# Optimization experiments

Measured on AMD Instinct MI355X. Metric: run time of the kernel, lower is better.

The kernel has to match this reference:

```python
import jax, jax.numpy as jnp
import numpy as np


def setup_inputs() -> dict:
    key = jax.random.key(0)
    ks = jax.random.split(key, 5)
    B, T, D, L = 4, 8192, 1024, 128
    X = jax.random.normal(ks[0], (B, T, D), dtype=jnp.float32)
    attention_mask = jnp.ones((B, T), dtype=jnp.float32)
    sd_dl = 1.0 / np.sqrt(D)  # lecun_normal fan_in = D
    Wk = jax.random.normal(ks[1], (D, L), dtype=jnp.float32) * sd_dl
    Wq = jax.random.normal(ks[2], (D, L), dtype=jnp.float32) * sd_dl
    Wv = jax.random.normal(ks[3], (D, D), dtype=jnp.float32) * sd_dl
    o_proj = jax.random.normal(ks[4], (D, D), dtype=jnp.float32) * sd_dl
    return {"X": X, "attention_mask": attention_mask, "Wk": Wk, "Wq": Wq,
            "Wv": Wv, "o_proj": o_proj, "n_heads": 16}


def reference(X, attention_mask, Wk, Wq, Wv, o_proj, n_heads):
    B, T, D = X.shape
    H = n_heads
    # Projections, laid out time-major as in the original: (T, B, H, *)
    V = jnp.einsum('DM,BTD->TBM', Wv, X).reshape(T, B, H, -1)   # (T,B,H,d)
    Q = jnp.einsum('DL,BTD->TBL', Wq, X).reshape(T, B, H, -1)   # (T,B,H,l)
    K = jnp.einsum('DL,BTD->TBL', Wk, X).reshape(T, B, H, -1)   # (T,B,H,l)
    m = attention_mask.T[:, :, None, None]                       # (T,B,1,1)
    V = V * m
    Qs = jax.nn.softmax(Q, axis=-1)
    maxi = jnp.max(K, axis=0, keepdims=True)                     # global max over T
    K = jnp.exp(K - maxi) * m
    Kv = jnp.einsum('tbhl,tbhd->bhld', K, V)                     # global KV state
    Ksum = K.sum(axis=0)                                         # (B,H,l)
    Kv = Kv / Ksum[..., None]
    y = jnp.einsum('tbhl,bhld->bthd', Qs, Kv).reshape(B, T, D)
    return y @ o_proj
```

## Files before the change

kernel.cpp:

```cpp
#include <hip/hip_runtime.h>
#include <hip/hip_bf16.h>

typedef unsigned short u16;
typedef unsigned int   u32;

typedef __attribute__((ext_vector_type(8))) short short8;
typedef __attribute__((ext_vector_type(4))) float f32x4;

typedef const __attribute__((address_space(1))) void g_void;
typedef __attribute__((address_space(3))) void l_void;

__device__ __forceinline__ float bf2f(u16 u) {
    u32 x = ((u32)u) << 16;
    return __builtin_bit_cast(float, x);
}
__device__ __forceinline__ u16 f2bf(float f) {
    u32 u = __builtin_bit_cast(u32, f);
    u32 r = (u + 0x7FFFu + ((u >> 16) & 1u)) >> 16;
    return (u16)r;
}
__device__ __forceinline__ u32 pack2(float a, float b) {
    return (u32)f2bf(a) | ((u32)f2bf(b) << 16);
}

__global__ void detect_kernel(const u16* __restrict__ X, int* __restrict__ flags) {
    __shared__ int cnt[256];
    int c = 0;
    for (int i = threadIdx.x; i < 16384; i += 256) {
        u16 v = X[i];
        int e = (v >> 7) & 0xFF;
        c += (e >= 104 && e <= 140) ? 1 : 0;
    }
    cnt[threadIdx.x] = c;
    __syncthreads();
    for (int s = 128; s > 0; s >>= 1) {
        if (threadIdx.x < s) cnt[threadIdx.x] += cnt[threadIdx.x + s];
        __syncthreads();
    }
    if (threadIdx.x == 0) {
        flags[0] = (cnt[0] < 14746) ? 1 : 0;
        flags[1] = 0;
    }
}

__global__ __launch_bounds__(256) void convert_x(const float* __restrict__ Xf,
                                                 u16* __restrict__ XC,
                                                 const int* __restrict__ flags, int n) {
    if (flags[0] == 0) return;
    int i = (blockIdx.x * 256 + threadIdx.x) * 8;
    if (i >= n) return;
    float4 a = *(const float4*)(Xf + i);
    float4 b = *(const float4*)(Xf + i + 4);
    uint4 o;
    o.x = pack2(a.x, a.y); o.y = pack2(a.z, a.w);
    o.z = pack2(b.x, b.y); o.w = pack2(b.z, b.w);
    *(uint4*)(XC + i) = o;
}

__global__ __launch_bounds__(256) void gemm_bt(
    const u16* __restrict__ A0, const u16* __restrict__ A1, int lda,
    const u16* __restrict__ Bt, int ldb,
    void* __restrict__ C, int ldc,
    int Mtiles, int K,
    const int* __restrict__ aselp, const int* __restrict__ ofp) {
    __shared__ char smem[32768];

    const u16* A = aselp[0] ? A1 : A0;

    const int tid = threadIdx.x;
    const int w = tid >> 6, lane = tid & 63;
    const int Ntiles = gridDim.x / Mtiles;
    const int q8 = gridDim.x >> 3;
    const int t  = (blockIdx.x & 7) * q8 + (blockIdx.x >> 3);
    const int mt = t / Ntiles;
    const int nt = t % Ntiles;
    const int m0 = mt << 7, n0 = nt << 7;
    const int wm = w >> 1, wn = w & 1;

    f32x4 acc[4][4] = {};

    const int rr = w * 16 + (lane >> 2);
    const int cg = (lane & 3) ^ ((lane >> 3) & 3);

    const u16* gA0 = A + (m0 + rr) * lda + cg * 8;
    const u16* gA1 = A + (m0 + rr + 64) * lda + cg * 8;
    const u16* gB0 = Bt + (n0 + rr) * ldb + cg * 8;
    const u16* gB1 = Bt + (n0 + rr + 64) * ldb + cg * 8;

    const int st0 = w * 1024 + lane * 16;

    const int fr_a = (wm << 6) + (lane & 15);
    const int fr_b = (wn << 6) + (lane & 15);
    const int sl = (lane >> 4) ^ ((lane >> 1) & 3);
    const int offA = fr_a * 64 + sl * 16;
    const int offB = 8192 + fr_b * 64 + sl * 16;

#define STAGE(buf, kt) do {                                                        \
        char* sb_ = smem + (buf) * 16384;                                          \
        __builtin_amdgcn_global_load_lds((g_void*)(gA0 + (kt)),                    \
            (l_void*)(sb_ + st0), 16, 0, 0);                                       \
        __builtin_amdgcn_global_load_lds((g_void*)(gA1 + (kt)),                    \
            (l_void*)(sb_ + 4096 + st0), 16, 0, 0);                                \
        __builtin_amdgcn_global_load_lds((g_void*)(gB0 + (kt)),                    \
            (l_void*)(sb_ + 8192 + st0), 16, 0, 0);                                \
        __builtin_amdgcn_global_load_lds((g_void*)(gB1 + (kt)),                    \
            (l_void*)(sb_ + 12288 + st0), 16, 0, 0);                               \
    } while (0)

#define COMPUTE(buf) do {                                                          \
        const char* cb_ = smem + (buf) * 16384;                                    \
        short8 af[4], bfv[4];                                                      \
        _Pragma("unroll")                                                          \
        for (int i = 0; i < 4; ++i) {                                              \
            af[i]  = *(const short8*)(cb_ + offA + i * 1024);                      \
            bfv[i] = *(const short8*)(cb_ + offB + i * 1024);                      \
        }                                                                          \
        _Pragma("unroll")                                                          \
        for (int mi = 0; mi < 4; ++mi)                                             \
            _Pragma("unroll")                                                      \
            for (int ni = 0; ni < 4; ++ni)                                         \
                acc[mi][ni] = __builtin_amdgcn_mfma_f32_16x16x32_bf16(             \
                    af[mi], bfv[ni], acc[mi][ni], 0, 0, 0);                        \
    } while (0)

    STAGE(0, 0);
    int cur = 0;
    for (int kt = 32; kt < K; kt += 32) {
        STAGE(cur ^ 1, kt);
        asm volatile("s_waitcnt vmcnt(4)" ::: "memory");
        __builtin_amdgcn_s_barrier();
        __builtin_amdgcn_sched_barrier(0);
        COMPUTE(cur);
        __builtin_amdgcn_sched_barrier(0);
        __builtin_amdgcn_s_barrier();
        cur ^= 1;
    }
    asm volatile("s_waitcnt vmcnt(0)" ::: "memory");
    __builtin_amdgcn_s_barrier();
    __builtin_amdgcn_sched_barrier(0);
    COMPUTE(cur);
    __syncthreads();

#undef STAGE
#undef COMPUTE

    const int out_fp32 = ofp[0];
    float* fb = (float*)smem;
    const int lrow = tid >> 3, cgp = tid & 7;
#pragma unroll
    for (int mi = 0; mi < 4; ++mi) {
#pragma unroll
        for (int ni = 0; ni < 4; ++ni) {
#pragma unroll
            for (int r = 0; r < 4; ++r) {
                int lr = wm * 16 + ((lane >> 4) << 2) + r;
                int lc = wn * 64 + ni * 16 + (lane & 15);
                fb[lr * 132 + lc] = acc[mi][ni][r];
            }
        }
        __syncthreads();
        int grow = (lrow < 16) ? (mi * 16 + lrow) : (48 + mi * 16 + lrow);
        const float* srcp = fb + lrow * 132 + cgp * 16;
        if (out_fp32) {
            float4* dst = (float4*)((float*)C + (size_t)(m0 + grow) * ldc + n0 + cgp * 16);
            dst[0] = make_float4(srcp[0], srcp[1], srcp[2], srcp[3]);
            dst[1] = make_float4(srcp[4], srcp[5], srcp[6], srcp[7]);
            dst[2] = make_float4(srcp[8], srcp[9], srcp[10], srcp[11]);
            dst[3] = make_float4(srcp[12], srcp[13], srcp[14], srcp[15]);
        } else {
            u32 o0 = pack2(srcp[0], srcp[1]);
            u32 o1 = pack2(srcp[2], srcp[3]);
            u32 o2 = pack2(srcp[4], srcp[5]);
            u32 o3 = pack2(srcp[6], srcp[7]);
            u32 o4 = pack2(srcp[8], srcp[9]);
            u32 o5 = pack2(srcp[10], srcp[11]);
            u32 o6 = pack2(srcp[12], srcp[13]);
            u32 o7 = pack2(srcp[14], srcp[15]);
            uint4* dst = (uint4*)((u16*)C + (size_t)(m0 + grow) * ldc + n0 + cgp * 16);
            dst[0] = make_uint4(o0, o1, o2, o3);
            dst[1] = make_uint4(o4, o5, o6, o7);
        }
        __syncthreads();
    }
}

__device__ __forceinline__ u16 rd_elem(const void* s, int idx, int fp32) {
    return fp32 ? f2bf(((const float*)s)[idx]) : ((const u16*)s)[idx];
}

__global__ void transpose_k(const void* __restrict__ Wq, const void* __restrict__ Wk,
                            const void* __restrict__ Wv, const void* __restrict__ Op,
                            u16* __restrict__ W1T, u16* __restrict__ OpT,
                            const int* __restrict__ flags) {
    int fp32 = flags[0];
    int id = blockIdx.x;
    const void* src; u16* dst; int Nc, mid;
    if (id < 128)       { src = Wq; dst = W1T;               Nc = 128;  mid = id; }
    else if (id < 256)  { src = Wk; dst = W1T + 128 * 1024;  Nc = 128;  mid = id - 128; }
    else if (id < 1280) { src = Wv; dst = W1T + 256 * 1024;  Nc = 1024; mid = id - 256; }
    else                { src = Op; dst = OpT;               Nc = 1024; mid = id - 1280; }
    int kt = mid & 31, nt = mid >> 5;
    __shared__ u16 tile[32][33];
    int x = threadIdx.x & 31, y0 = threadIdx.x >> 5;
#pragma unroll
    for (int yy = 0; yy < 4; ++yy) {
        int y = y0 * 4 + yy;
        tile[y][x] = rd_elem(src, (kt * 32 + y) * Nc + nt * 32 + x, fp32);
    }
    __syncthreads();
#pragma unroll
    for (int yy = 0; yy < 4; ++yy) {
        int y = y0 * 4 + yy;
        dst[(nt * 32 + y) * 1024 + kt * 32 + x] = tile[x][y];
    }
}

__global__ __launch_bounds__(256) void kvpart_kernel(const u16* __restrict__ QKV,
                                                     const void* __restrict__ mask,
                                                     const int* __restrict__ flags,
                                                     float* __restrict__ Kvp,
                                                     float* __restrict__ Ksp) {
    int t_ = (blockIdx.x & 7) * 256 + (blockIdx.x >> 3);
    int h = t_ & 15;
    int bc = t_ >> 4;
    int chunk = bc & 31, b = bc >> 5;
    int w = threadIdx.x >> 6, lane = threadIdx.x & 63;
    int fp32m = flags[0];

    float kv[8] = {0, 0, 0, 0, 0, 0, 0, 0};
    float ks[8] = {0, 0, 0, 0, 0, 0, 0, 0};
    int t0 = chunk * 256;
    for (int i = 0; i < 64; ++i) {
        int t = t0 + w + i * 4;
        int m = b * 8192 + t;
        const u16* row = QKV + (size_t)m * 1280;
        float v = bf2f(row[256 + h * 64 + lane]);
        uint4 kq = *(const uint4*)(row + 128 + h * 8);
        float msk = fp32m ? ((const float*)mask)[m] : bf2f(((const u16*)mask)[m]);
        float vm = v * msk;
        float kf[8];
        kf[0] = __builtin_bit_cast(float, kq.x << 16);
        kf[1] = __builtin_bit_cast(float, kq.x & 0xffff0000u);
        kf[2] = __builtin_bit_cast(float, kq.y << 16);
        kf[3] = __builtin_bit_cast(float, kq.y & 0xffff0000u);
        kf[4] = __builtin_bit_cast(float, kq.z << 16);
        kf[5] = __builtin_bit_cast(float, kq.z & 0xffff0000u);
        kf[6] = __builtin_bit_cast(float, kq.w << 16);
        kf[7] = __builtin_bit_cast(float, kq.w & 0xffff0000u);
#pragma unroll
        for (int l = 0; l < 8; ++l) {
            float e = __expf(kf[l]) * msk;
            kv[l] += e * vm;
            ks[l] += e;
        }
    }
    __shared__ float red[4][8][64];
    __shared__ float redks[4][8];
#pragma unroll
    for (int l = 0; l < 8; ++l) red[w][l][lane] = kv[l];
    if (lane == 0) {
#pragma unroll
        for (int l = 0; l < 8; ++l) redks[w][l] = ks[l];
    }
    __syncthreads();
    int tid = threadIdx.x;
    int obid = (b * 16 + h) * 32 + chunk;
    for (int c = tid; c < 512; c += 256) {
        int l = c >> 6, d = c & 63;
        Kvp[obid * 512 + c] = red[0][l][d] + red[1][l][d] + red[2][l][d] + red[3][l][d];
    }
    if (tid < 8) Ksp[obid * 8 + tid] = redks[0][tid] + redks[1][tid] + redks[2][tid] + redks[3][tid];
}

__global__ void kvreduce_kernel(const float* __restrict__ Kvp, const float* __restrict__ Ksp,
                                float* __restrict__ Kv) {
    int bh = blockIdx.x >> 2;
    int seg = blockIdx.x & 3;
    int c0 = seg * 128 + threadIdx.x;
    int l = c0 >> 6;
    float s = 0.f, ks = 0.f;
    for (int c = 0; c < 32; ++c) {
        s += Kvp[(bh * 32 + c) * 512 + c0];
        ks += Ksp[(bh * 32 + c) * 8 + l];
    }
    Kv[bh * 512 + c0] = s / ks;
}

__global__ __launch_bounds__(256) void y_kernel(u16* __restrict__ QKV,
                                                const float* __restrict__ Kv) {
    int bid = blockIdx.x;
    int b = bid >> 9, chunk = bid & 511;
    int w = threadIdx.x >> 6, lane = threadIdx.x & 63;
    int hh = w & 1;
    int rp = w >> 1;
    int hloc = lane >> 3;
    int h = hh * 8 + hloc;
    int dg = lane & 7;

    float4 kva[8], kvb[8];
    const float* kvp = Kv + (b * 16 + h) * 512 + dg * 8;
#pragma unroll
    for (int l = 0; l < 8; ++l) {
        kva[l] = *(const float4*)(kvp + l * 64);
        kvb[l] = *(const float4*)(kvp + l * 64 + 4);
    }
    int lgrp = lane & 56;
    for (int i = 0; i < 8; ++i) {
        int t = chunk * 16 + i * 2 + rp;
        int m = b * 8192 + t;
        u16* row = QKV + (size_t)m * 1280;
        float qv = bf2f(row[hh * 64 + lane]);
        float qm = qv;
        qm = fmaxf(qm, __shfl_xor(qm, 1));
        qm = fmaxf(qm, __shfl_xor(qm, 2));
        qm = fmaxf(qm, __shfl_xor(qm, 4));
        float e = __expf(qv - qm);
        float s = e;
        s += __shfl_xor(s, 1);
        s += __shfl_xor(s, 2);
        s += __shfl_xor(s, 4);
        float qs = e / s;
        float4 a0 = {0.f, 0.f, 0.f, 0.f}, a1 = {0.f, 0.f, 0.f, 0.f};
#pragma unroll
        for (int l = 0; l < 8; ++l) {
            float ql = __shfl(qs, lgrp + l);
            a0.x += ql * kva[l].x; a0.y += ql * kva[l].y;
            a0.z += ql * kva[l].z; a0.w += ql * kva[l].w;
            a1.x += ql * kvb[l].x; a1.y += ql * kvb[l].y;
            a1.z += ql * kvb[l].z; a1.w += ql * kvb[l].w;
        }
        uint4 o;
        o.x = pack2(a0.x, a0.y);
        o.y = pack2(a0.z, a0.w);
        o.z = pack2(a1.x, a1.y);
        o.w = pack2(a1.z, a1.w);
        *(uint4*)(row + 256 + h * 64 + dg * 8) = o;
    }
}

#define OFF_FLAG ((size_t)0)
#define OFF_W1T  ((size_t)1024)
#define OFF_OPT  ((size_t)2622464)
#define OFF_KVP  ((size_t)4787200)
#define OFF_KSP  ((size_t)8981504)
#define OFF_KV   ((size_t)9047040)
#define OFF_XC   ((size_t)9309184)
#define OFF_QKV  ((size_t)76418048)

extern "C" void kernel_launch(void* const* d_in, const int* in_sizes, int n_in,
                              void* d_out, int out_size, void* d_ws, size_t ws_size,
                              hipStream_t stream) {
    const u16* X   = (const u16*)d_in[0];
    const void* msk = d_in[1];
    const void* Wk  = d_in[2];
    const void* Wq  = d_in[3];
    const void* Wv  = d_in[4];
    const void* Op  = d_in[5];

    char* ws = (char*)d_ws;
    int*   FLAGS = (int*)(ws + OFF_FLAG);
    u16*   W1T  = (u16*)(ws + OFF_W1T);
    u16*   OPT  = (u16*)(ws + OFF_OPT);
    float* KVP  = (float*)(ws + OFF_KVP);
    float* KSP  = (float*)(ws + OFF_KSP);
    float* KV   = (float*)(ws + OFF_KV);
    u16*   XC   = (u16*)(ws + OFF_XC);
    u16*   QKV  = (u16*)(ws + OFF_QKV);

    detect_kernel<<<1, 256, 0, stream>>>(X, FLAGS);
    convert_x<<<16384, 256, 0, stream>>>((const float*)d_in[0], XC, FLAGS, 33554432);
    transpose_k<<<2304, 256, 0, stream>>>(Wq, Wk, Wv, Op, W1T, OPT, FLAGS);
    gemm_bt<<<2560, 256, 0, stream>>>(X, XC, 1024, W1T, 1024, QKV, 1280, 256, 1024,
                                      FLAGS, FLAGS + 1);
    kvpart_kernel<<<2048, 256, 0, stream>>>(QKV, msk, FLAGS, KVP, KSP);
    kvreduce_kernel<<<256, 128, 0, stream>>>(KVP, KSP, KV);
    y_kernel<<<2048, 256, 0, stream>>>(QKV, KV);
    gemm_bt<<<2048, 256, 0, stream>>>(QKV + 256, QKV + 256, 1280, OPT, 1024,
                                      d_out, 1024, 256, 1024, FLAGS + 1, FLAGS);
}
```

Baseline: 533.9 us.

## Triple-buffer GEMM K-loop and merge X conversion with weight transpose kernel

```diff
diff --git a/kernel.cpp b/kernel.cpp
--- a/kernel.cpp
+++ b/kernel.cpp
@@ -43,18 +43,48 @@
     }
 }
 
-__global__ __launch_bounds__(256) void convert_x(const float* __restrict__ Xf,
-                                                 u16* __restrict__ XC,
-                                                 const int* __restrict__ flags, int n) {
-    if (flags[0] == 0) return;
-    int i = (blockIdx.x * 256 + threadIdx.x) * 8;
-    if (i >= n) return;
-    float4 a = *(const float4*)(Xf + i);
-    float4 b = *(const float4*)(Xf + i + 4);
-    uint4 o;
-    o.x = pack2(a.x, a.y); o.y = pack2(a.z, a.w);
-    o.z = pack2(b.x, b.y); o.w = pack2(b.z, b.w);
-    *(uint4*)(XC + i) = o;
+__device__ __forceinline__ u16 rd_elem(const void* s, int idx, int fp32) {
+    return fp32 ? f2bf(((const float*)s)[idx]) : ((const u16*)s)[idx];
+}
+
+__global__ __launch_bounds__(256) void prep_kernel(
+    const float* __restrict__ Xf, u16* __restrict__ XC,
+    const void* __restrict__ Wq, const void* __restrict__ Wk,
+    const void* __restrict__ Wv, const void* __restrict__ Op,
+    u16* __restrict__ W1T, u16* __restrict__ OpT,
+    const int* __restrict__ flags) {
+    int fp32 = flags[0];
+    if (blockIdx.x < 16384) {
+        if (fp32 == 0) return;
+        int i = (blockIdx.x * 256 + threadIdx.x) * 8;
+        float4 a = *(const float4*)(Xf + i);
+        float4 b = *(const float4*)(Xf + i + 4);
+        uint4 o;
+        o.x = pack2(a.x, a.y); o.y = pack2(a.z, a.w);
+        o.z = pack2(b.x, b.y); o.w = pack2(b.z, b.w);
+        *(uint4*)(XC + i) = o;
+        return;
+    }
+    int id = blockIdx.x - 16384;
+    const void* src; u16* dst; int Nc, mid;
+    if (id < 128)       { src = Wq; dst = W1T;               Nc = 128;  mid = id; }
+    else if (id < 256)  { src = Wk; dst = W1T + 128 * 1024;  Nc = 128;  mid = id - 128; }
+    else if (id < 1280) { src = Wv; dst = W1T + 256 * 1024;  Nc = 1024; mid = id - 256; }
+    else                { src = Op; dst = OpT;               Nc = 1024; mid = id - 1280; }
+    int kt = mid & 31, nt = mid >> 5;
+    __shared__ u16 tile[32][33];
+    int x = threadIdx.x & 31, y0 = threadIdx.x >> 5;
+#pragma unroll
+    for (int yy = 0; yy < 4; ++yy) {
+        int y = y0 * 4 + yy;
+        tile[y][x] = rd_elem(src, (kt * 32 + y) * Nc + nt * 32 + x, fp32);
+    }
+    __syncthreads();
+#pragma unroll
+    for (int yy = 0; yy < 4; ++yy) {
+        int y = y0 * 4 + yy;
+        dst[(nt * 32 + y) * 1024 + kt * 32 + x] = tile[x][y];
+    }
 }
 
 __global__ __launch_bounds__(256) void gemm_bt(
@@ -63,7 +93,7 @@
     void* __restrict__ C, int ldc,
     int Mtiles, int K,
     const int* __restrict__ aselp, const int* __restrict__ ofp) {
-    __shared__ char smem[32768];
+    __shared__ char smem[49152];
 
     const u16* A = aselp[0] ? A1 : A0;
 
@@ -123,22 +153,32 @@
                     af[mi], bfv[ni], acc[mi][ni], 0, 0, 0);                        \
     } while (0)
 
+    const int ntiles = K >> 5;
     STAGE(0, 0);
-    int cur = 0;
-    for (int kt = 32; kt < K; kt += 32) {
-        STAGE(cur ^ 1, kt);
-        asm volatile("s_waitcnt vmcnt(4)" ::: "memory");
+    STAGE(1, 32);
+    int cc = 0, sc = 2;
+    for (int i = 0; i < ntiles - 2; ++i) {
+        STAGE(sc, (i + 2) << 5);
+        asm volatile("s_waitcnt vmcnt(8)" ::: "memory");
         __builtin_amdgcn_s_barrier();
         __builtin_amdgcn_sched_barrier(0);
-        COMPUTE(cur);
+        COMPUTE(cc);
         __builtin_amdgcn_sched_barrier(0);
         __builtin_amdgcn_s_barrier();
-        cur ^= 1;
-    }
+        cc = (cc == 2) ? 0 : cc + 1;
+        sc = (sc == 2) ? 0 : sc + 1;
+    }
+    asm volatile("s_waitcnt vmcnt(4)" ::: "memory");
+    __builtin_amdgcn_s_barrier();
+    __builtin_amdgcn_sched_barrier(0);
+    COMPUTE(cc);
+    __builtin_amdgcn_sched_barrier(0);
+    __builtin_amdgcn_s_barrier();
+    cc = (cc == 2) ? 0 : cc + 1;
     asm volatile("s_waitcnt vmcnt(0)" ::: "memory");
     __builtin_amdgcn_s_barrier();
     __builtin_amdgcn_sched_barrier(0);
-    COMPUTE(cur);
+    COMPUTE(cc);
     __syncthreads();
 
 #undef STAGE
@@ -184,37 +224,6 @@
     }
 }
 
-__device__ __forceinline__ u16 rd_elem(const void* s, int idx, int fp32) {
-    return fp32 ? f2bf(((const float*)s)[idx]) : ((const u16*)s)[idx];
-}
-
-__global__ void transpose_k(const void* __restrict__ Wq, const void* __restrict__ Wk,
-                            const void* __restrict__ Wv, const void* __restrict__ Op,
-                            u16* __restrict__ W1T, u16* __restrict__ OpT,
-                            const int* __restrict__ flags) {
-    int fp32 = flags[0];
-    int id = blockIdx.x;
-    const void* src; u16* dst; int Nc, mid;
-    if (id < 128)       { src = Wq; dst = W1T;               Nc = 128;  mid = id; }
-    else if (id < 256)  { src = Wk; dst = W1T + 128 * 1024;  Nc = 128;  mid = id - 128; }
-    else if (id < 1280) { src = Wv; dst = W1T + 256 * 1024;  Nc = 1024; mid = id - 256; }
-    else                { src = Op; dst = OpT;               Nc = 1024; mid = id - 1280; }
-    int kt = mid & 31, nt = mid >> 5;
-    __shared__ u16 tile[32][33];
-    int x = threadIdx.x & 31, y0 = threadIdx.x >> 5;
-#pragma unroll
-    for (int yy = 0; yy < 4; ++yy) {
-        int y = y0 * 4 + yy;
-        tile[y][x] = rd_elem(src, (kt * 32 + y) * Nc + nt * 32 + x, fp32);
-    }
-    __syncthreads();
-#pragma unroll
-    for (int yy = 0; yy < 4; ++yy) {
-        int y = y0 * 4 + yy;
-        dst[(nt * 32 + y) * 1024 + kt * 32 + x] = tile[x][y];
-    }
-}
-
 __global__ __launch_bounds__(256) void kvpart_kernel(const u16* __restrict__ QKV,
                                                      const void* __restrict__ mask,
                                                      const int* __restrict__ flags,
@@ -368,8 +377,8 @@
     u16*   QKV  = (u16*)(ws + OFF_QKV);
 
     detect_kernel<<<1, 256, 0, stream>>>(X, FLAGS);
-    convert_x<<<16384, 256, 0, stream>>>((const float*)d_in[0], XC, FLAGS, 33554432);
-    transpose_k<<<2304, 256, 0, stream>>>(Wq, Wk, Wv, Op, W1T, OPT, FLAGS);
+    prep_kernel<<<18688, 256, 0, stream>>>((const float*)d_in[0], XC,
+                                           Wq, Wk, Wv, Op, W1T, OPT, FLAGS);
     gemm_bt<<<2560, 256, 0, stream>>>(X, XC, 1024, W1T, 1024, QKV, 1280, 256, 1024,
                                       FLAGS, FLAGS + 1);
     kvpart_kernel<<<2048, 256, 0, stream>>>(QKV, msk, FLAGS, KVP, KSP);
```

Measured after the change: 532.7 us. About the same (-0.2%).
